# Performance work log

Measured on AMD Instinct MI355X. Metric: run time of the kernel, lower is better.

## Reference

```python
import jax, jax.numpy as jnp
import numpy as np

EMB_W, COMMIT_W, ENT_W = 1.0, 0.25, 0.1  # loss weights from init_kwargs


def setup_inputs() -> dict:
    key = jax.random.key(0)
    k1, k2 = jax.random.split(key)
    B, H, W, D, K = 32, 32, 32, 64, 1024
    inputs = jax.random.normal(k1, (B, H, W, D), dtype=jnp.float32)
    # keras RandomUniform default: U(-0.05, 0.05)
    codebook = jax.random.uniform(k2, (K, D), dtype=jnp.float32, minval=-0.05, maxval=0.05)
    return {"inputs": inputs, "codebook": codebook}


def reference(inputs, codebook):
    # inputs: [B,H,W,D], codebook: [K,D]
    D = inputs.shape[-1]
    x = inputs.reshape(-1, D)  # [N,D]
    dist = (
        jnp.sum(x * x, axis=-1, keepdims=True)
        - 2.0 * (x @ codebook.T)
        + jnp.sum(codebook * codebook, axis=-1)
    )  # [N,K]
    tokens = jnp.argmin(dist, axis=-1)  # [N]
    emb = codebook[tokens].reshape(inputs.shape)  # [B,H,W,D]

    embedding_loss = EMB_W * jnp.mean((jax.lax.stop_gradient(emb) - inputs) ** 2)
    commitment_loss = COMMIT_W * jnp.mean((emb - jax.lax.stop_gradient(inputs)) ** 2)
    # 'entropy' loss as written in call(): mean over codebook of per-code min distance
    entropy_loss = ENT_W * jnp.mean(jnp.min(dist, axis=0))
    loss = embedding_loss + commitment_loss + entropy_loss

    # training=True path: straight-through estimator
    out = inputs + jax.lax.stop_gradient(emb - inputs)
    return out, loss
```

## Files before the change

### kernel.cpp

```cpp
#include <hip/hip_runtime.h>
#include <math.h>

#define NROWS 32768
#define NCODE 1024
#define AMB_CAP 8192
#define GAP_THRESH 1.5e-4f

typedef __attribute__((ext_vector_type(8))) short bf16x8;
typedef __attribute__((ext_vector_type(4))) float f32x4;

__device__ __forceinline__ unsigned short bf16_rne(float f) {
    unsigned u = __float_as_uint(f);
    unsigned r = u + 0x7FFFu + ((u >> 16) & 1u);
    return (unsigned short)(r >> 16);
}

__global__ __launch_bounds__(64) void vq_prep(
    const float* __restrict__ cb, float* __restrict__ cn4,
    unsigned* __restrict__ minK, unsigned* __restrict__ counter,
    float* __restrict__ gsumsq, unsigned* __restrict__ ticket,
    unsigned short* __restrict__ wsB)
{
    int c = blockIdx.x * 64 + threadIdx.x;
    if (c == 0) { *counter = 0u; *gsumsq = 0.f; *ticket = 0u; }
    float v[64];
    const float4* src = (const float4*)(cb + (size_t)c * 64);
    float s = 0.f;
    #pragma unroll
    for (int i = 0; i < 16; i++) {
        float4 t = src[i];
        v[i*4+0] = t.x; v[i*4+1] = t.y; v[i*4+2] = t.z; v[i*4+3] = t.w;
        s += t.x*t.x + t.y*t.y + t.z*t.z + t.w*t.w;
    }
    cn4[c] = s + 4.0f;
    minK[c] = 0x7F800000u;
    int cc = c >> 6, ct = (c >> 4) & 3, cl = c & 15;
    #pragma unroll
    for (int q = 0; q < 4; q++) {
        int half = q & 1, lo = q >> 1;
        #pragma unroll
        for (int g = 0; g < 4; g++) {
            unsigned short u8[8] __attribute__((aligned(16)));
            #pragma unroll
            for (int j = 0; j < 8; j++) {
                float f = -2.0f * v[half*32 + g*8 + j];
                unsigned short h = bf16_rne(f);
                if (lo) h = bf16_rne(f - __uint_as_float((unsigned)h << 16));
                u8[j] = h;
            }
            size_t off = (size_t)cc * 8192 + ct * 2048 + q * 512 + (g * 16 + cl) * 8;
            *(uint4*)(wsB + off) = *(const uint4*)u8;
        }
    }
}

__global__ __launch_bounds__(512, 4) void vq_main(
    const float* __restrict__ x, const float* __restrict__ cb,
    const unsigned short* __restrict__ wsB, const float* __restrict__ cn4,
    float* __restrict__ out, unsigned* __restrict__ minK,
    unsigned* __restrict__ counter, int* __restrict__ amb,
    float* __restrict__ gsumsq)
{
    __shared__ float    cn4L[1024];
    __shared__ unsigned scrE[1024];
    __shared__ float mD1[128], mD2[128];
    __shared__ int   mI1[128];
    __shared__ int   tokS[64];
    __shared__ float redS[8];

    const int tid = threadIdx.x;
    const int lane = tid & 63;
    const int wi = tid >> 6;
    const int g = wi >> 1;
    const int h = wi & 1;
    const int ln15 = lane & 15;
    const int q = lane >> 4;
    const int row0 = blockIdx.x * 64;

    cn4L[tid]       = cn4[tid];
    cn4L[512 + tid] = cn4[512 + tid];
    scrE[tid]       = 0x7F800000u;
    scrE[512 + tid] = 0x7F800000u;

    bf16x8 Ah0, Ah1, Al0, Al1;
    float xnm4[4];
    {
        const float* xr = x + (size_t)(row0 + g*16 + ln15) * 64 + q * 8;
        float4 f0 = *(const float4*)xr;
        float4 f1 = *(const float4*)(xr + 4);
        float4 f2 = *(const float4*)(xr + 32);
        float4 f3 = *(const float4*)(xr + 36);
        float fa[8] = {f0.x,f0.y,f0.z,f0.w,f1.x,f1.y,f1.z,f1.w};
        float fb[8] = {f2.x,f2.y,f2.z,f2.w,f3.x,f3.y,f3.z,f3.w};
        unsigned short hh8[8] __attribute__((aligned(16)));
        unsigned short ll8[8] __attribute__((aligned(16)));
        unsigned short h28[8] __attribute__((aligned(16)));
        unsigned short l28[8] __attribute__((aligned(16)));
        float ss = 0.f;
        #pragma unroll
        for (int j = 0; j < 8; j++) {
            ss += fa[j]*fa[j] + fb[j]*fb[j];
            unsigned short hh = bf16_rne(fa[j]);
            hh8[j] = hh; ll8[j] = bf16_rne(fa[j] - __uint_as_float((unsigned)hh << 16));
            hh = bf16_rne(fb[j]);
            h28[j] = hh; l28[j] = bf16_rne(fb[j] - __uint_as_float((unsigned)hh << 16));
        }
        Ah0 = *(const bf16x8*)hh8; Al0 = *(const bf16x8*)ll8;
        Ah1 = *(const bf16x8*)h28; Al1 = *(const bf16x8*)l28;
        ss += __shfl_xor(ss, 16);
        ss += __shfl_xor(ss, 32);
        #pragma unroll
        for (int r = 0; r < 4; r++)
            xnm4[r] = __shfl(ss, (q << 2) | r, 64) - 4.0f;
    }
    __syncthreads();

    float d1[4], d2[4];
    int   i1[4];
    #pragma unroll
    for (int r = 0; r < 4; r++) { d1[r] = INFINITY; d2[r] = INFINITY; i1[r] = 0; }

    const char* wsQ = (const char*)wsB + (size_t)h * 131072 + lane * 16;
    #pragma unroll 4
    for (int t = 0; t < 32; t++) {
        const char* tb = wsQ + t * 4096;
        bf16x8 Bh0 = *(const bf16x8*)(tb);
        bf16x8 Bh1 = *(const bf16x8*)(tb + 1024);
        bf16x8 Bl0 = *(const bf16x8*)(tb + 2048);
        bf16x8 Bl1 = *(const bf16x8*)(tb + 3072);
        const int kid = h*512 + t*16 + ln15;
        const float cn4v = cn4L[kid];
        f32x4 a0 = {cn4v, cn4v, cn4v, cn4v};
        a0 = __builtin_amdgcn_mfma_f32_16x16x32_bf16(Ah0, Bh0, a0, 0, 0, 0);
        a0 = __builtin_amdgcn_mfma_f32_16x16x32_bf16(Ah1, Bh1, a0, 0, 0, 0);
        a0 = __builtin_amdgcn_mfma_f32_16x16x32_bf16(Ah0, Bl0, a0, 0, 0, 0);
        a0 = __builtin_amdgcn_mfma_f32_16x16x32_bf16(Ah1, Bl1, a0, 0, 0, 0);
        a0 = __builtin_amdgcn_mfma_f32_16x16x32_bf16(Al0, Bh0, a0, 0, 0, 0);
        a0 = __builtin_amdgcn_mfma_f32_16x16x32_bf16(Al1, Bh1, a0, 0, 0, 0);
        float cm = INFINITY;
        #pragma unroll
        for (int r = 0; r < 4; r++) {
            float wv = a0[r];
            bool lt = wv < d1[r];
            d2[r] = lt ? d1[r] : fminf(d2[r], wv);
            i1[r] = lt ? kid   : i1[r];
            d1[r] = lt ? wv    : d1[r];
            cm = fminf(cm, wv + xnm4[r]);
        }
        cm = fminf(cm, __shfl_xor(cm, 16));
        cm = fminf(cm, __shfl_xor(cm, 32));
        if (q == (t & 3)) atomicMin(&scrE[kid], __float_as_uint(cm));
    }

    #pragma unroll
    for (int d = 1; d < 16; d <<= 1) {
        #pragma unroll
        for (int r = 0; r < 4; r++) {
            float od1 = __shfl_xor(d1[r], d);
            int   oi1 = __shfl_xor(i1[r], d);
            float od2 = __shfl_xor(d2[r], d);
            bool take = (od1 < d1[r]) || (od1 == d1[r] && oi1 < i1[r]);
            float loser = take ? d1[r] : od1;
            d2[r] = fminf(fminf(d2[r], od2), loser);
            d1[r] = take ? od1 : d1[r];
            i1[r] = take ? oi1 : i1[r];
        }
    }
    if (ln15 == 0) {
        #pragma unroll
        for (int r = 0; r < 4; r++) {
            int idx = (g*16 + q*4 + r) * 2 + h;
            mD1[idx] = d1[r]; mI1[idx] = i1[r]; mD2[idx] = d2[r];
        }
    }
    __syncthreads();

    if (tid < 64) {
        float a1 = mD1[tid*2],   b1 = mD1[tid*2+1];
        int   ai = mI1[tid*2],   bi = mI1[tid*2+1];
        float a2 = mD2[tid*2],   b2 = mD2[tid*2+1];
        bool ta = (a1 < b1) || (a1 == b1 && ai < bi);
        float D1 = ta ? a1 : b1;
        int   I1 = ta ? ai : bi;
        float D2 = ta ? fminf(a2, b1) : fminf(b2, a1);
        tokS[tid] = I1;
        if (D2 - D1 < GAP_THRESH) {
            unsigned idx = atomicAdd(counter, 1u);
            if (idx < AMB_CAP) { amb[2*idx] = row0 + tid; amb[2*idx+1] = I1; }
        }
    }

    {
        unsigned u0 = scrE[tid];
        if (u0 < minK[tid]) atomicMin(&minK[tid], u0);
        unsigned u1 = scrE[512 + tid];
        if (u1 < minK[512 + tid]) atomicMin(&minK[512 + tid], u1);
    }
    __syncthreads();

    {
        float acc2 = 0.f;
        #pragma unroll
        for (int uu = 0; uu < 2; uu++) {
            int u = uu*512 + tid;
            int row = u >> 4, c4 = u & 15;
            int tok = tokS[row];
            float4 c = ((const float4*)(cb + (size_t)tok*64))[c4];
            float4 xx = ((const float4*)(x + (size_t)(row0 + row)*64))[c4];
            ((float4*)(out + (size_t)(row0 + row)*64))[c4] = c;
            float dx = c.x-xx.x, dy = c.y-xx.y, dz = c.z-xx.z, dw = c.w-xx.w;
            acc2 += dx*dx + dy*dy + dz*dz + dw*dw;
        }
        #pragma unroll
        for (int o = 32; o > 0; o >>= 1) acc2 += __shfl_down(acc2, o);
        if (lane == 0) redS[wi] = acc2;
        __syncthreads();
        if (tid == 0) {
            float t = 0.f;
            #pragma unroll
            for (int w = 0; w < 8; w++) t += redS[w];
            atomicAdd(gsumsq, t);
        }
    }
}

__global__ __launch_bounds__(256) void vq_tail(
    const float* __restrict__ x, const float* __restrict__ cb,
    float* __restrict__ out, const unsigned* __restrict__ counter,
    const int* __restrict__ amb, float* __restrict__ gsumsq,
    unsigned* __restrict__ ticket, const unsigned* __restrict__ minK,
    float* __restrict__ out_loss)
{
    __shared__ __align__(16) float cbS[16384];
    __shared__ double xs[64];
    __shared__ double bd[256];
    __shared__ int    bi[256];
    __shared__ unsigned lastS;
    __shared__ float redS[4];

    const int tid = threadIdx.x;

    unsigned cnt = *counter; if (cnt > AMB_CAP) cnt = AMB_CAP;
    for (unsigned i = blockIdx.x; i < cnt; i += gridDim.x) {
        int row = amb[2*i], oldk = amb[2*i+1];
        __syncthreads();
        if (tid < 64) xs[tid] = (double)x[(size_t)row*64 + tid];
        __syncthreads();
        double xn = 0.0;
        #pragma unroll 8
        for (int d = 0; d < 64; d++) xn += xs[d]*xs[d];
        double best = INFINITY; int bk = 1 << 30;
        for (int b = 0; b < 4; b++) {
            __syncthreads();
            #pragma unroll
            for (int k = 0; k < 16; k++)
                ((float4*)cbS)[k*256 + tid] = ((const float4*)cb)[b*4096 + k*256 + tid];
            __syncthreads();
            int kcode = b*256 + tid;
            const int t6 = tid & 63;
            double dot = 0.0, cn2 = 0.0;
            #pragma unroll 8
            for (int dd = 0; dd < 64; dd++) {
                int d = (dd + t6) & 63;
                double cv = (double)cbS[tid*64 + d];
                dot = fma(xs[d], cv, dot);
                cn2 = fma(cv, cv, cn2);
            }
            double dist = (xn - 2.0*dot) + cn2;
            if (dist < best || (dist == best && kcode < bk)) { best = dist; bk = kcode; }
        }
        bd[tid] = best; bi[tid] = bk;
        __syncthreads();
        for (int s = 128; s > 0; s >>= 1) {
            if (tid < s) {
                double od = bd[tid+s]; int ok = bi[tid+s];
                if (od < bd[tid] || (od == bd[tid] && ok < bi[tid])) { bd[tid] = od; bi[tid] = ok; }
            }
            __syncthreads();
        }
        int bestk = bi[0];
        if (bestk != oldk) {
            double part = 0.0;
            if (tid < 64) {
                float cn = cb[(size_t)bestk*64 + tid];
                float co = cb[(size_t)oldk*64 + tid];
                out[(size_t)row*64 + tid] = cn;
                double dn = (double)cn - xs[tid];
                double dl = (double)co - xs[tid];
                part = dn*dn - dl*dl;
            }
            __syncthreads();
            bd[tid] = part;
            __syncthreads();
            for (int s = 128; s > 0; s >>= 1) {
                if (tid < s) bd[tid] += bd[tid+s];
                __syncthreads();
            }
            if (tid == 0) atomicAdd(gsumsq, (float)bd[0]);
        }
    }

    __syncthreads();
    if (tid == 0) {
        __threadfence();
        lastS = (atomicAdd(ticket, 1u) == 63u) ? 1u : 0u;
    }
    __syncthreads();
    if (lastS) {
        __threadfence();
        float s = 0.f;
        #pragma unroll
        for (int jj = 0; jj < 4; jj++)
            s += __uint_as_float(minK[jj*256 + tid]);
        #pragma unroll
        for (int o = 32; o > 0; o >>= 1) s += __shfl_down(s, o);
        if ((tid & 63) == 0) redS[tid >> 6] = s;
        __syncthreads();
        if (tid == 0) {
            float gs = atomicAdd(gsumsq, 0.0f);
            float tot = redS[0] + redS[1] + redS[2] + redS[3];
            out_loss[0] = 1.25f * (gs / 2097152.0f) + 0.1f * (tot / 1024.0f);
        }
    }
}

extern "C" void kernel_launch(void* const* d_in, const int* in_sizes, int n_in,
                              void* d_out, int out_size, void* d_ws, size_t ws_size,
                              hipStream_t stream) {
    const float* x  = (const float*)d_in[0];
    const float* cb = (const float*)d_in[1];
    float* out = (float*)d_out;

    char* ws = (char*)d_ws;
    unsigned*       counter = (unsigned*)ws;
    float*          gsumsq  = (float*)(ws + 4);
    unsigned*       ticket  = (unsigned*)(ws + 8);
    float*          cn4     = (float*)(ws + 1024);
    unsigned*       minK    = (unsigned*)(ws + 8192);
    int*            amb     = (int*)(ws + 16384);
    unsigned short* wsB     = (unsigned short*)(ws + 131072);

    vq_prep<<<16,  64,  0, stream>>>(cb, cn4, minK, counter, gsumsq, ticket, wsB);
    vq_main<<<512, 512, 0, stream>>>(x, cb, wsB, cn4, out, minK, counter, amb, gsumsq);
    vq_tail<<<64,  256, 0, stream>>>(x, cb, out, counter, amb, gsumsq, ticket, minK,
                                     out + 2097152);
}
```

Measured before the change: 112.7 us.

## Halve rows per block and split codebook across four waves per row group

Each block of vq_main now handles 32 rows instead of 64, with four waves each scanning a quarter of the codebook instead of two waves each scanning half. The grid doubles to 1024 blocks and launch bounds ask for 8 blocks per CU. The aim is more parallelism and occupancy with shorter serial MFMA loops. The top-2 update becomes branch-free min/max, and the per-code min reduction drops its cross-lane shuffles in favour of an LDS atomicMin from every lane. In exchange, codebook B-fragments are reloaded twice as often per row and the LDS atomic traffic goes up, while the tighter register budget may cause spills.

```diff
diff --git a/kernel.cpp b/kernel.cpp
--- a/kernel.cpp
+++ b/kernel.cpp
@@ -54,7 +54,7 @@
     }
 }
 
-__global__ __launch_bounds__(512, 4) void vq_main(
+__global__ __launch_bounds__(512, 8) void vq_main(
     const float* __restrict__ x, const float* __restrict__ cb,
     const unsigned short* __restrict__ wsB, const float* __restrict__ cn4,
     float* __restrict__ out, unsigned* __restrict__ minK,
@@ -65,17 +65,17 @@
     __shared__ unsigned scrE[1024];
     __shared__ float mD1[128], mD2[128];
     __shared__ int   mI1[128];
-    __shared__ int   tokS[64];
+    __shared__ int   tokS[32];
     __shared__ float redS[8];
 
     const int tid = threadIdx.x;
     const int lane = tid & 63;
     const int wi = tid >> 6;
-    const int g = wi >> 1;
-    const int h = wi & 1;
+    const int rg = wi >> 2;
+    const int h2 = wi & 3;
     const int ln15 = lane & 15;
     const int q = lane >> 4;
-    const int row0 = blockIdx.x * 64;
+    const int row0 = blockIdx.x * 32;
 
     cn4L[tid]       = cn4[tid];
     cn4L[512 + tid] = cn4[512 + tid];
@@ -85,7 +85,7 @@
     bf16x8 Ah0, Ah1, Al0, Al1;
     float xnm4[4];
     {
-        const float* xr = x + (size_t)(row0 + g*16 + ln15) * 64 + q * 8;
+        const float* xr = x + (size_t)(row0 + rg*16 + ln15) * 64 + q * 8;
         float4 f0 = *(const float4*)xr;
         float4 f1 = *(const float4*)(xr + 4);
         float4 f2 = *(const float4*)(xr + 32);
@@ -120,15 +120,15 @@
     #pragma unroll
     for (int r = 0; r < 4; r++) { d1[r] = INFINITY; d2[r] = INFINITY; i1[r] = 0; }
 
-    const char* wsQ = (const char*)wsB + (size_t)h * 131072 + lane * 16;
-    #pragma unroll 4
-    for (int t = 0; t < 32; t++) {
+    const char* wsQ = (const char*)wsB + (size_t)h2 * 65536 + lane * 16;
+    #pragma unroll 2
+    for (int t = 0; t < 16; t++) {
         const char* tb = wsQ + t * 4096;
         bf16x8 Bh0 = *(const bf16x8*)(tb);
         bf16x8 Bh1 = *(const bf16x8*)(tb + 1024);
         bf16x8 Bl0 = *(const bf16x8*)(tb + 2048);
         bf16x8 Bl1 = *(const bf16x8*)(tb + 3072);
-        const int kid = h*512 + t*16 + ln15;
+        const int kid = h2*256 + t*16 + ln15;
         const float cn4v = cn4L[kid];
         f32x4 a0 = {cn4v, cn4v, cn4v, cn4v};
         a0 = __builtin_amdgcn_mfma_f32_16x16x32_bf16(Ah0, Bh0, a0, 0, 0, 0);
@@ -141,15 +141,13 @@
         #pragma unroll
         for (int r = 0; r < 4; r++) {
             float wv = a0[r];
+            d2[r] = fminf(fmaxf(wv, d1[r]), d2[r]);
             bool lt = wv < d1[r];
-            d2[r] = lt ? d1[r] : fminf(d2[r], wv);
-            i1[r] = lt ? kid   : i1[r];
-            d1[r] = lt ? wv    : d1[r];
+            i1[r] = lt ? kid : i1[r];
+            d1[r] = fminf(wv, d1[r]);
             cm = fminf(cm, wv + xnm4[r]);
         }
-        cm = fminf(cm, __shfl_xor(cm, 16));
-        cm = fminf(cm, __shfl_xor(cm, 32));
-        if (q == (t & 3)) atomicMin(&scrE[kid], __float_as_uint(cm));
+        atomicMin(&scrE[kid], __float_as_uint(cm));
     }
 
     #pragma unroll
@@ -169,20 +167,24 @@
     if (ln15 == 0) {
         #pragma unroll
         for (int r = 0; r < 4; r++) {
-            int idx = (g*16 + q*4 + r) * 2 + h;
+            int idx = (rg*16 + q*4 + r) * 4 + h2;
             mD1[idx] = d1[r]; mI1[idx] = i1[r]; mD2[idx] = d2[r];
         }
     }
     __syncthreads();
 
-    if (tid < 64) {
-        float a1 = mD1[tid*2],   b1 = mD1[tid*2+1];
-        int   ai = mI1[tid*2],   bi = mI1[tid*2+1];
-        float a2 = mD2[tid*2],   b2 = mD2[tid*2+1];
-        bool ta = (a1 < b1) || (a1 == b1 && ai < bi);
-        float D1 = ta ? a1 : b1;
-        int   I1 = ta ? ai : bi;
-        float D2 = ta ? fminf(a2, b1) : fminf(b2, a1);
+    if (tid < 32) {
+        float D1 = mD1[tid*4]; int I1 = mI1[tid*4]; float D2 = mD2[tid*4];
+        #pragma unroll
+        for (int j = 1; j < 4; j++) {
+            float b1 = mD1[tid*4 + j];
+            int   bi = mI1[tid*4 + j];
+            float b2 = mD2[tid*4 + j];
+            bool ta = (D1 < b1) || (D1 == b1 && I1 < bi);
+            float loser = ta ? b1 : D1;
+            D2 = fminf(fminf(D2, b2), loser);
+            if (!ta) { D1 = b1; I1 = bi; }
+        }
         tokS[tid] = I1;
         if (D2 - D1 < GAP_THRESH) {
             unsigned idx = atomicAdd(counter, 1u);
@@ -199,18 +201,13 @@
     __syncthreads();
 
     {
-        float acc2 = 0.f;
-        #pragma unroll
-        for (int uu = 0; uu < 2; uu++) {
-            int u = uu*512 + tid;
-            int row = u >> 4, c4 = u & 15;
-            int tok = tokS[row];
-            float4 c = ((const float4*)(cb + (size_t)tok*64))[c4];
-            float4 xx = ((const float4*)(x + (size_t)(row0 + row)*64))[c4];
-            ((float4*)(out + (size_t)(row0 + row)*64))[c4] = c;
-            float dx = c.x-xx.x, dy = c.y-xx.y, dz = c.z-xx.z, dw = c.w-xx.w;
-            acc2 += dx*dx + dy*dy + dz*dz + dw*dw;
-        }
+        int row = tid >> 4, c4 = tid & 15;
+        int tok = tokS[row];
+        float4 c = ((const float4*)(cb + (size_t)tok*64))[c4];
+        float4 xx = ((const float4*)(x + (size_t)(row0 + row)*64))[c4];
+        ((float4*)(out + (size_t)(row0 + row)*64))[c4] = c;
+        float dx = c.x-xx.x, dy = c.y-xx.y, dz = c.z-xx.z, dw = c.w-xx.w;
+        float acc2 = dx*dx + dy*dy + dz*dz + dw*dw;
         #pragma unroll
         for (int o = 32; o > 0; o >>= 1) acc2 += __shfl_down(acc2, o);
         if (lane == 0) redS[wi] = acc2;
@@ -340,8 +337,8 @@
     int*            amb     = (int*)(ws + 16384);
     unsigned short* wsB     = (unsigned short*)(ws + 131072);
 
-    vq_prep<<<16,  64,  0, stream>>>(cb, cn4, minK, counter, gsumsq, ticket, wsB);
-    vq_main<<<512, 512, 0, stream>>>(x, cb, wsB, cn4, out, minK, counter, amb, gsumsq);
-    vq_tail<<<64,  256, 0, stream>>>(x, cb, out, counter, amb, gsumsq, ticket, minK,
-                                     out + 2097152);
-}
+    vq_prep<<<16,   64,  0, stream>>>(cb, cn4, minK, counter, gsumsq, ticket, wsB);
+    vq_main<<<1024, 512, 0, stream>>>(x, cb, wsB, cn4, out, minK, counter, amb, gsumsq);
+    vq_tail<<<64,   256, 0, stream>>>(x, cb, out, counter, amb, gsumsq, ticket, minK,
+                                      out + 2097152);
+}
```

Measured after the change: 122.6 us. +8.8%, slower.
